# Kernel optimization log

Measured on AMD Instinct MI355X. Metric: run time of the kernel, lower is better.

The kernel has to match this reference:

```python
import jax, jax.numpy as jnp
import numpy as np

TOKENS = 8192
IN_FEATURES = 4096
OUT_FEATURES = 4096
ALPHA = 2e-05
BETA = 8.0


def setup_inputs() -> dict:
    key = jax.random.key(0)
    kx, kw = jax.random.split(key)
    # int8 activations and weights, values in [-127, 127]
    x = jax.random.randint(kx, (TOKENS, IN_FEATURES), -127, 128, dtype=jnp.int32).astype(jnp.int8)
    weight = jax.random.randint(kw, (OUT_FEATURES, IN_FEATURES), -127, 128, dtype=jnp.int32).astype(jnp.int8)
    bias = jnp.zeros((OUT_FEATURES,), dtype=jnp.float32)
    a = jnp.float32(ALPHA)  # dequant scale: input_scale * weight_scale
    b = jnp.float32(BETA)   # requant scale: 1 / out_scale
    return {"x": x, "weight": weight, "bias": bias, "a": a, "b": b}


def reference(x, weight, bias, a, b):
    acc = jnp.matmul(x.astype(jnp.int32), weight.T.astype(jnp.int32))
    # fp32 epilogue: dequant scale + bias, exact GeLU, requant by beta
    y = a * acc.astype(jnp.float32) + bias[None, :]
    y = jax.nn.gelu(y, approximate=False)
    # quantize output to int8 (round to nearest even, saturate)
    q = jnp.clip(jnp.rint(y * b), -128.0, 127.0).astype(jnp.int8)
    return q
```

## Files before the change

kernel.cpp:

```cpp
#include <hip/hip_runtime.h>
#include <cstdint>
#include <cstddef>

#define TOKENS 8192
#define INF    4096
#define OUTF   4096

typedef int v4i __attribute__((ext_vector_type(4)));

__global__ __launch_bounds__(256) void pack_i8_kernel(
    const int* __restrict__ xi, const int* __restrict__ wi,
    uint8_t* __restrict__ x8, uint8_t* __restrict__ w8) {
  const int NXT = (TOKENS * INF) / 16;
  const int NT  = 2048 * 256;
  int tid = blockIdx.x * 256 + threadIdx.x;
#pragma unroll 1
  for (int g = 0; g < 6; ++g) {
    int t = g * NT + tid;
    const int4* s;
    int4* d;
    if (t < NXT) {
      s = (const int4*)xi + 4 * (size_t)t;
      d = (int4*)x8 + t;
    } else {
      int t2 = t - NXT;
      s = (const int4*)wi + 4 * (size_t)t2;
      d = (int4*)w8 + t2;
    }
    int4 v0 = s[0], v1 = s[1], v2 = s[2], v3 = s[3];
    int4 p;
    p.x = (v0.x & 255) | ((v0.y & 255) << 8) | ((v0.z & 255) << 16) | (v0.w << 24);
    p.y = (v1.x & 255) | ((v1.y & 255) << 8) | ((v1.z & 255) << 16) | (v1.w << 24);
    p.z = (v2.x & 255) | ((v2.y & 255) << 8) | ((v2.z & 255) << 16) | (v2.w << 24);
    p.w = (v3.x & 255) | ((v3.y & 255) << 8) | ((v3.z & 255) << 16) | (v3.w << 24);
    *d = p;
  }
}

__device__ __forceinline__ float gelu_exact(float y) {
  float x = y * 0.70710678118654752f;
  float s = fabsf(x);
  float t = __builtin_amdgcn_rcpf(fmaf(s, 0.3275911f, 1.0f));
  float p = t * fmaf(t, fmaf(t, fmaf(t, fmaf(t, 1.061405429f, -1.453152027f),
                                     1.421413741f), -0.284496736f),
                     0.254829592f);
  float e = __expf(-s * s);
  float er = fmaf(-p, e, 1.0f);
  er = copysignf(er, x);
  return 0.5f * y * (1.0f + er);
}

__device__ __forceinline__ void barrier_fenced() {
  asm volatile("" ::: "memory");
  __builtin_amdgcn_s_barrier();
  asm volatile("" ::: "memory");
}

__global__ __launch_bounds__(512, 2) void gemm_i8_gelu_q_kernel(
    const uint8_t* __restrict__ x8, const uint8_t* __restrict__ w8,
    const float* __restrict__ bias, const float* __restrict__ pa,
    const float* __restrict__ pb, int* __restrict__ out) {
  __shared__ char sm[131072];

  const int tid = threadIdx.x;
  const int l   = tid & 63;
  const int wv  = tid >> 6;
  const int wr  = wv >> 2;
  const int wc  = wv & 3;
  const int lr  = l & 15;
  const int lg  = l >> 4;

  int id = blockIdx.x;
  int wg = (id & 7) * 64 + (id >> 3);
  const int m0 = (wg >> 4) * 256;
  const int n0 = (wg & 15) * 256;

  const float av = pa[0];
  const float bv = pb[0];

  const int grow = (wv << 5) + (l >> 3);
  const int gch  = ((l & 7) ^ ((l >> 3) & 7)) << 4;
  const uint8_t* gA = x8 + (size_t)(m0 + grow) * INF + gch;
  const uint8_t* gB = w8 + (size_t)(n0 + grow) * INF + gch;
  const int dwv = wv * 4096;

  int aoff[8], boff[4], sb0, sb1;
#pragma unroll
  for (int m = 0; m < 8; ++m) aoff[m] = (wr * 128 + m * 16 + lr) * 128;
#pragma unroll
  for (int n = 0; n < 4; ++n) boff[n] = 32768 + (wc * 64 + n * 16 + lr) * 128;
  sb0 = ((0 + lg) ^ (l & 7)) << 4;
  sb1 = ((4 + lg) ^ (l & 7)) << 4;

  v4i acc[8][4];
#pragma unroll
  for (int m = 0; m < 8; ++m)
#pragma unroll
    for (int n = 0; n < 4; ++n) acc[m][n] = (v4i){0, 0, 0, 0};

#define GLL(gsrc, ldst)                                                       \
  __builtin_amdgcn_global_load_lds(                                           \
      (const __attribute__((address_space(1))) unsigned*)(gsrc),              \
      (__attribute__((address_space(3))) unsigned*)(ldst), 16, 0, 0);

#define GLA(T, J) GLL(gA + (size_t)(J) * 8 * INF + (size_t)(T) * 128,         \
                      sm + (((T) & 1) << 16) + dwv + (J) * 1024)
#define GLB(T, J) GLL(gB + (size_t)(J) * 8 * INF + (size_t)(T) * 128,         \
                      sm + (((T) & 1) << 16) + 32768 + dwv + (J) * 1024)

#define LD(off) (*(const v4i*)(sbr + (off)))
#define MM(ACC, AF, BF)                                                       \
  ACC = __builtin_amdgcn_mfma_i32_16x16x64_i8(AF, BF, ACC, 0, 0, 0)

#define CL(AF, BF, MB, NB)                                                    \
  __builtin_amdgcn_s_setprio(1);                                              \
  MM(acc[(MB)+0][(NB)+0], AF[0], BF[0]); MM(acc[(MB)+0][(NB)+1], AF[0], BF[1]);\
  MM(acc[(MB)+1][(NB)+0], AF[1], BF[0]); MM(acc[(MB)+1][(NB)+1], AF[1], BF[1]);\
  MM(acc[(MB)+2][(NB)+0], AF[2], BF[0]); MM(acc[(MB)+2][(NB)+1], AF[2], BF[1]);\
  MM(acc[(MB)+3][(NB)+0], AF[3], BF[0]); MM(acc[(MB)+3][(NB)+1], AF[3], BF[1]);\
  __builtin_amdgcn_s_setprio(0);

#define ITER(DS)                                                              \
  {                                                                           \
    const char* sbr = sm + ((kt & 1) << 16);                                  \
    const int T = kt + 1;                                                     \
    asm volatile("s_waitcnt vmcnt(0)" ::: "memory");      \
    barrier_fenced();           \
    if (DS) {                                                                 \
      GLA(T, 0); GLA(T, 1); GLA(T, 2); GLA(T, 3);                             \
      GLB(T, 0); GLB(T, 1); GLB(T, 2); GLB(T, 3);                             \
    }                                                                         \
    v4i a0[4], a4[4], b0[2], b2[2];                             \
    v4i c0[4], c4[4], d0[2], d2[2];             \
    a0[0] = LD(aoff[0] + sb0); a0[1] = LD(aoff[1] + sb0);                     \
    a0[2] = LD(aoff[2] + sb0); a0[3] = LD(aoff[3] + sb0);                     \
    b0[0] = LD(boff[0] + sb0); b0[1] = LD(boff[1] + sb0);                     \
    a4[0] = LD(aoff[4] + sb0); a4[1] = LD(aoff[5] + sb0);                     \
    a4[2] = LD(aoff[6] + sb0); a4[3] = LD(aoff[7] + sb0);                     \
    b2[0] = LD(boff[2] + sb0); b2[1] = LD(boff[3] + sb0);                     \
    CL(a0, b0, 0, 0)                                                          \
    c0[0] = LD(aoff[0] + sb1); c0[1] = LD(aoff[1] + sb1);                     \
    c0[2] = LD(aoff[2] + sb1); c0[3] = LD(aoff[3] + sb1);                     \
    d0[0] = LD(boff[0] + sb1); d0[1] = LD(boff[1] + sb1);                     \
    CL(a4, b0, 4, 0)                                                          \
    CL(a0, b2, 0, 2)                                                          \
    c4[0] = LD(aoff[4] + sb1); c4[1] = LD(aoff[5] + sb1);                     \
    c4[2] = LD(aoff[6] + sb1); c4[3] = LD(aoff[7] + sb1);                     \
    d2[0] = LD(boff[2] + sb1); d2[1] = LD(boff[3] + sb1);                     \
    CL(a4, b2, 4, 2)                                                          \
    CL(c0, d0, 0, 0)                                                          \
    CL(c4, d0, 4, 0)                                                          \
    CL(c0, d2, 0, 2)                                                          \
    CL(c4, d2, 4, 2)                                                          \
     \
    if (DS) { __builtin_amdgcn_sched_group_barrier(0x020, 8, 0); }            \
    __builtin_amdgcn_sched_group_barrier(0x100, 12, 0);                       \
    __builtin_amdgcn_sched_group_barrier(0x008, 8, 0);                        \
    __builtin_amdgcn_sched_group_barrier(0x100, 6, 0);                        \
    __builtin_amdgcn_sched_group_barrier(0x008, 16, 0);                       \
    __builtin_amdgcn_sched_group_barrier(0x100, 6, 0);                        \
    __builtin_amdgcn_sched_group_barrier(0x008, 40, 0);                       \
  }

  GLA(0, 0); GLA(0, 1); GLA(0, 2); GLA(0, 3);
  GLB(0, 0); GLB(0, 1); GLB(0, 2); GLB(0, 3);

#pragma unroll 1
  for (int kt = 0; kt < 31; ++kt) ITER(1)
  {
    const int kt = 31;
    ITER(0)
  }

  float bvals[4];
#pragma unroll
  for (int n = 0; n < 4; ++n) bvals[n] = bias[n0 + wc * 64 + n * 16 + lr];

#pragma unroll
  for (int m = 0; m < 8; ++m) {
    int rowb = m0 + wr * 128 + m * 16 + lg * 4;
#pragma unroll
    for (int q = 0; q < 4; ++q) {
      size_t rb = (size_t)(rowb + q) * OUTF;
#pragma unroll
      for (int n = 0; n < 4; ++n) {
        float f = fmaf(av, (float)acc[m][n][q], bvals[n]);
        float g = gelu_exact(f);
        float r = __builtin_rintf(g * bv);
        r = fminf(fmaxf(r, -128.0f), 127.0f);
        out[rb + (size_t)(n0 + wc * 64 + n * 16 + lr)] = (int)r;
      }
    }
  }
#undef GLL
#undef GLA
#undef GLB
#undef LD
#undef MM
#undef CL
#undef ITER
}

extern "C" void kernel_launch(void* const* d_in, const int* in_sizes, int n_in,
                              void* d_out, int out_size, void* d_ws,
                              size_t ws_size, hipStream_t stream) {
  const int*   xi   = (const int*)d_in[0];
  const int*   wi   = (const int*)d_in[1];
  const float* bias = (const float*)d_in[2];
  const float* pa   = (const float*)d_in[3];
  const float* pb   = (const float*)d_in[4];
  int*         out  = (int*)d_out;

  uint8_t* x8 = (uint8_t*)d_ws;
  uint8_t* w8 = x8 + (size_t)TOKENS * INF;

  pack_i8_kernel<<<2048, 256, 0, stream>>>(xi, wi, x8, w8);

  dim3 grid((TOKENS / 256) * (OUTF / 256));
  gemm_i8_gelu_q_kernel<<<grid, 512, 0, stream>>>(x8, w8, bias, pa, pb, out);
}
```

Before: 385.6 us.

## Use 4 waves per block with 128x128 per-wave tiles

Shrinks the GEMM workgroup from 8 waves to 4, so each wave now computes a 128x128 output sub-tile (8x8 MFMA accumulators) instead of 128x64. Each wave issues twice as many global-to-LDS loads per k-step, and the sched_group_barrier interleaving of LDS reads and MFMAs is rewritten to match. The aim is more MFMA work per LDS fragment read and fewer waves sharing each barrier. The cost is 256 accumulator registers per lane, which limits occupancy to one block per CU and raises the risk of register spills.

```diff
diff --git a/kernel.cpp b/kernel.cpp
--- a/kernel.cpp
+++ b/kernel.cpp
@@ -56,7 +56,7 @@
   asm volatile("" ::: "memory");
 }
 
-__global__ __launch_bounds__(512, 2) void gemm_i8_gelu_q_kernel(
+__global__ __launch_bounds__(256, 1) void gemm_i8_gelu_q_kernel(
     const uint8_t* __restrict__ x8, const uint8_t* __restrict__ w8,
     const float* __restrict__ bias, const float* __restrict__ pa,
     const float* __restrict__ pb, int* __restrict__ out) {
@@ -65,8 +65,8 @@
   const int tid = threadIdx.x;
   const int l   = tid & 63;
   const int wv  = tid >> 6;
-  const int wr  = wv >> 2;
-  const int wc  = wv & 3;
+  const int wr  = wv >> 1;
+  const int wc  = wv & 1;
   const int lr  = l & 15;
   const int lg  = l >> 4;
 
@@ -78,25 +78,25 @@
   const float av = pa[0];
   const float bv = pb[0];
 
-  const int grow = (wv << 5) + (l >> 3);
+  const int grow = (wv << 6) + (l >> 3);
   const int gch  = ((l & 7) ^ ((l >> 3) & 7)) << 4;
   const uint8_t* gA = x8 + (size_t)(m0 + grow) * INF + gch;
   const uint8_t* gB = w8 + (size_t)(n0 + grow) * INF + gch;
-  const int dwv = wv * 4096;
-
-  int aoff[8], boff[4], sb0, sb1;
+  const int dwv = wv * 8192;
+
+  int aoff[8], boff[8], sb0, sb1;
 #pragma unroll
   for (int m = 0; m < 8; ++m) aoff[m] = (wr * 128 + m * 16 + lr) * 128;
 #pragma unroll
-  for (int n = 0; n < 4; ++n) boff[n] = 32768 + (wc * 64 + n * 16 + lr) * 128;
+  for (int n = 0; n < 8; ++n) boff[n] = 32768 + (wc * 128 + n * 16 + lr) * 128;
   sb0 = ((0 + lg) ^ (l & 7)) << 4;
   sb1 = ((4 + lg) ^ (l & 7)) << 4;
 
-  v4i acc[8][4];
+  v4i acc[8][8];
 #pragma unroll
   for (int m = 0; m < 8; ++m)
 #pragma unroll
-    for (int n = 0; n < 4; ++n) acc[m][n] = (v4i){0, 0, 0, 0};
+    for (int n = 0; n < 8; ++n) acc[m][n] = (v4i){0, 0, 0, 0};
 
 #define GLL(gsrc, ldst)                                                       \
   __builtin_amdgcn_global_load_lds(                                           \
@@ -111,59 +111,59 @@
 #define LD(off) (*(const v4i*)(sbr + (off)))
 #define MM(ACC, AF, BF)                                                       \
   ACC = __builtin_amdgcn_mfma_i32_16x16x64_i8(AF, BF, ACC, 0, 0, 0)
-
-#define CL(AF, BF, MB, NB)                                                    \
-  __builtin_amdgcn_s_setprio(1);                                              \
-  MM(acc[(MB)+0][(NB)+0], AF[0], BF[0]); MM(acc[(MB)+0][(NB)+1], AF[0], BF[1]);\
-  MM(acc[(MB)+1][(NB)+0], AF[1], BF[0]); MM(acc[(MB)+1][(NB)+1], AF[1], BF[1]);\
-  MM(acc[(MB)+2][(NB)+0], AF[2], BF[0]); MM(acc[(MB)+2][(NB)+1], AF[2], BF[1]);\
-  MM(acc[(MB)+3][(NB)+0], AF[3], BF[0]); MM(acc[(MB)+3][(NB)+1], AF[3], BF[1]);\
-  __builtin_amdgcn_s_setprio(0);
+#define SGB(m, n) __builtin_amdgcn_sched_group_barrier((m), (n), 0)
 
 #define ITER(DS)                                                              \
   {                                                                           \
     const char* sbr = sm + ((kt & 1) << 16);                                  \
     const int T = kt + 1;                                                     \
     asm volatile("s_waitcnt vmcnt(0)" ::: "memory");      \
-    barrier_fenced();           \
+    barrier_fenced();                      \
     if (DS) {                                                                 \
       GLA(T, 0); GLA(T, 1); GLA(T, 2); GLA(T, 3);                             \
+      GLA(T, 4); GLA(T, 5); GLA(T, 6); GLA(T, 7);                             \
       GLB(T, 0); GLB(T, 1); GLB(T, 2); GLB(T, 3);                             \
+      GLB(T, 4); GLB(T, 5); GLB(T, 6); GLB(T, 7);                             \
     }                                                                         \
-    v4i a0[4], a4[4], b0[2], b2[2];                             \
-    v4i c0[4], c4[4], d0[2], d2[2];             \
-    a0[0] = LD(aoff[0] + sb0); a0[1] = LD(aoff[1] + sb0);                     \
-    a0[2] = LD(aoff[2] + sb0); a0[3] = LD(aoff[3] + sb0);                     \
-    b0[0] = LD(boff[0] + sb0); b0[1] = LD(boff[1] + sb0);                     \
-    a4[0] = LD(aoff[4] + sb0); a4[1] = LD(aoff[5] + sb0);                     \
-    a4[2] = LD(aoff[6] + sb0); a4[3] = LD(aoff[7] + sb0);                     \
-    b2[0] = LD(boff[2] + sb0); b2[1] = LD(boff[3] + sb0);                     \
-    CL(a0, b0, 0, 0)                                                          \
-    c0[0] = LD(aoff[0] + sb1); c0[1] = LD(aoff[1] + sb1);                     \
-    c0[2] = LD(aoff[2] + sb1); c0[3] = LD(aoff[3] + sb1);                     \
-    d0[0] = LD(boff[0] + sb1); d0[1] = LD(boff[1] + sb1);                     \
-    CL(a4, b0, 4, 0)                                                          \
-    CL(a0, b2, 0, 2)                                                          \
-    c4[0] = LD(aoff[4] + sb1); c4[1] = LD(aoff[5] + sb1);                     \
-    c4[2] = LD(aoff[6] + sb1); c4[3] = LD(aoff[7] + sb1);                     \
-    d2[0] = LD(boff[2] + sb1); d2[1] = LD(boff[3] + sb1);                     \
-    CL(a4, b2, 4, 2)                                                          \
-    CL(c0, d0, 0, 0)                                                          \
-    CL(c4, d0, 4, 0)                                                          \
-    CL(c0, d2, 0, 2)                                                          \
-    CL(c4, d2, 4, 2)                                                          \
-     \
-    if (DS) { __builtin_amdgcn_sched_group_barrier(0x020, 8, 0); }            \
-    __builtin_amdgcn_sched_group_barrier(0x100, 12, 0);                       \
-    __builtin_amdgcn_sched_group_barrier(0x008, 8, 0);                        \
-    __builtin_amdgcn_sched_group_barrier(0x100, 6, 0);                        \
-    __builtin_amdgcn_sched_group_barrier(0x008, 16, 0);                       \
-    __builtin_amdgcn_sched_group_barrier(0x100, 6, 0);                        \
-    __builtin_amdgcn_sched_group_barrier(0x008, 40, 0);                       \
+    v4i a[8], b[8], c[8], d[8];                                               \
+    _Pragma("unroll")                                                         \
+    for (int i = 0; i < 8; ++i) a[i] = LD(aoff[i] + sb0);                     \
+    _Pragma("unroll")                                                         \
+    for (int i = 0; i < 8; ++i) b[i] = LD(boff[i] + sb0);                     \
+                                               \
+    _Pragma("unroll")                                                         \
+    for (int m = 0; m < 4; ++m)                                               \
+      _Pragma("unroll")                                                       \
+      for (int n = 0; n < 8; ++n) MM(acc[m][n], a[m], b[n]);                  \
+                           \
+    _Pragma("unroll")                                                         \
+    for (int m = 4; m < 8; ++m) {                                             \
+      _Pragma("unroll")                                                       \
+      for (int n = 0; n < 8; ++n) MM(acc[m][n], a[m], b[n]);                  \
+      c[2 * (m - 4) + 0] = LD(aoff[2 * (m - 4) + 0] + sb1);                   \
+      c[2 * (m - 4) + 1] = LD(aoff[2 * (m - 4) + 1] + sb1);                   \
+      d[2 * (m - 4) + 0] = LD(boff[2 * (m - 4) + 0] + sb1);                   \
+      d[2 * (m - 4) + 1] = LD(boff[2 * (m - 4) + 1] + sb1);                   \
+    }                                                                         \
+                                                                      \
+    _Pragma("unroll")                                                         \
+    for (int m = 0; m < 8; ++m)                                               \
+      _Pragma("unroll")                                                       \
+      for (int n = 0; n < 8; ++n) MM(acc[m][n], c[m], d[n]);                  \
+         \
+    SGB(0x100, 16);                                                           \
+    SGB(0x008, 32);                                                           \
+    SGB(0x008, 8); SGB(0x100, 4);                                             \
+    SGB(0x008, 8); SGB(0x100, 4);                                             \
+    SGB(0x008, 8); SGB(0x100, 4);                                             \
+    SGB(0x008, 8); SGB(0x100, 4);                                             \
+    SGB(0x008, 64);                                                           \
   }
 
   GLA(0, 0); GLA(0, 1); GLA(0, 2); GLA(0, 3);
+  GLA(0, 4); GLA(0, 5); GLA(0, 6); GLA(0, 7);
   GLB(0, 0); GLB(0, 1); GLB(0, 2); GLB(0, 3);
+  GLB(0, 4); GLB(0, 5); GLB(0, 6); GLB(0, 7);
 
 #pragma unroll 1
   for (int kt = 0; kt < 31; ++kt) ITER(1)
@@ -172,9 +172,9 @@
     ITER(0)
   }
 
-  float bvals[4];
-#pragma unroll
-  for (int n = 0; n < 4; ++n) bvals[n] = bias[n0 + wc * 64 + n * 16 + lr];
+  float bvals[8];
+#pragma unroll
+  for (int n = 0; n < 8; ++n) bvals[n] = bias[n0 + wc * 128 + n * 16 + lr];
 
 #pragma unroll
   for (int m = 0; m < 8; ++m) {
@@ -183,12 +183,12 @@
     for (int q = 0; q < 4; ++q) {
       size_t rb = (size_t)(rowb + q) * OUTF;
 #pragma unroll
-      for (int n = 0; n < 4; ++n) {
+      for (int n = 0; n < 8; ++n) {
         float f = fmaf(av, (float)acc[m][n][q], bvals[n]);
         float g = gelu_exact(f);
         float r = __builtin_rintf(g * bv);
         r = fminf(fmaxf(r, -128.0f), 127.0f);
-        out[rb + (size_t)(n0 + wc * 64 + n * 16 + lr)] = (int)r;
+        out[rb + (size_t)(n0 + wc * 128 + n * 16 + lr)] = (int)r;
       }
     }
   }
@@ -197,7 +197,7 @@
 #undef GLB
 #undef LD
 #undef MM
-#undef CL
+#undef SGB
 #undef ITER
 }
 
@@ -217,5 +217,5 @@
   pack_i8_kernel<<<2048, 256, 0, stream>>>(xi, wi, x8, w8);
 
   dim3 grid((TOKENS / 256) * (OUTF / 256));
-  gemm_i8_gelu_q_kernel<<<grid, 512, 0, stream>>>(x8, w8, bias, pa, pb, out);
-}
+  gemm_i8_gelu_q_kernel<<<grid, 256, 0, stream>>>(x8, w8, bias, pa, pb, out);
+}
```

After: 432.4 us. +12.2%, slower.
